# Optimization experiments

Hardware: AMD Instinct MI355X
Metric: run time of the kernel (lower is better)

## Reference

```python
import jax, jax.numpy as jnp
import numpy as np

RGB2GRAY = jnp.array([0.299, 0.587, 0.114], dtype=jnp.float32)


def _trilinear_slice(grid, z, y, x):
    """grid: (F, L, GH, GW); z,y,x: (H, W) float positions in index space
    (align_corners=True convention). Returns (H, W, F)."""
    F_, L, GH, GW = grid.shape
    z = jnp.clip(z, 0.0, L - 1)
    y = jnp.clip(y, 0.0, GH - 1)
    x = jnp.clip(x, 0.0, GW - 1)
    z0 = jnp.floor(z).astype(jnp.int32); z1 = jnp.minimum(z0 + 1, L - 1)
    y0 = jnp.floor(y).astype(jnp.int32); y1 = jnp.minimum(y0 + 1, GH - 1)
    x0 = jnp.floor(x).astype(jnp.int32); x1 = jnp.minimum(x0 + 1, GW - 1)
    wz = (z - z0)[..., None]  # (H, W, 1)
    wy = (y - y0)[..., None]
    wx = (x - x0)[..., None]

    def g(zi, yi, xi):  # gather corner -> (H, W, F)
        return jnp.moveaxis(grid[:, zi, yi, xi], 0, -1)

    c00 = g(z0, y0, x0) * (1 - wx) + g(z0, y0, x1) * wx
    c01 = g(z0, y1, x0) * (1 - wx) + g(z0, y1, x1) * wx
    c10 = g(z1, y0, x0) * (1 - wx) + g(z1, y0, x1) * wx
    c11 = g(z1, y1, x0) * (1 - wx) + g(z1, y1, x1) * wx
    c0 = c00 * (1 - wy) + c01 * wy
    c1 = c10 * (1 - wy) + c11 * wy
    return c0 * (1 - wz) + c1 * wz


def setup_inputs() -> dict:
    key = jax.random.key(0)
    k = jax.random.split(key, 5)
    H, W = 1080, 1920
    N, F_, L, GH, GW = 50, 16, 8, 16, 16
    hidden = 64
    rgb = jax.random.uniform(k[0], (H, W, 3), dtype=jnp.float32)
    grids = jax.random.normal(k[1], (N, F_, L, GH, GW), dtype=jnp.float32) * 0.1
    W1 = jax.random.normal(k[2], (hidden, F_), dtype=jnp.float32) * (1.0 / np.sqrt(F_))
    W2 = jax.random.normal(k[3], (hidden, hidden), dtype=jnp.float32) * (1.0 / np.sqrt(hidden))
    W3 = jax.random.normal(k[4], (12, hidden), dtype=jnp.float32) * (1.0 / np.sqrt(hidden))
    return {"rgb": rgb, "grids": grids, "W1": W1, "W2": W2, "W3": W3, "cam_idx": 3}


def reference(rgb, grids, W1, W2, W3, cam_idx):
    H, W, _ = rgb.shape
    _, F_, L, GH, GW = grids.shape
    grid = grids[cam_idx]  # (F, L, GH, GW)
    # guidance: gray in [0,1]; grid_sample coords in [-1,1] with align_corners=True
    # map directly to index space: pos = coord01 * (size - 1)
    gray = jnp.clip(jnp.tensordot(rgb, RGB2GRAY, axes=([-1], [0])), 0.0, 1.0)  # (H, W)
    gy = jnp.linspace(0.0, 1.0, H, dtype=jnp.float32)[:, None]  # (H, 1)
    gx = jnp.linspace(0.0, 1.0, W, dtype=jnp.float32)[None, :]  # (1, W)
    z = gray * (L - 1)
    y = jnp.broadcast_to(gy * (GH - 1), (H, W))
    x = jnp.broadcast_to(gx * (GW - 1), (H, W))
    feat = _trilinear_slice(grid, z, y, x)  # (H, W, F)
    # tiny per-pixel MLP (bias-free, torch Linear applies x @ W.T)
    h = jnp.tanh(feat @ W1.T)
    h = jnp.tanh(h @ W2.T)
    out = h @ W3.T  # (H, W, 12)
    return out.reshape(1, H, W, 3, 4)
```

## Files before the change

### kernel.cpp

```cpp
#include <hip/hip_runtime.h>

#define H_IMG 1080
#define W_IMG 1920
#define NPIX (H_IMG * W_IMG)

typedef __attribute__((ext_vector_type(8))) short bfrag8;
typedef __attribute__((ext_vector_type(4))) float facc4;

#define PK2_OFF 131072
#define PK3_OFF 147456
#define PK1_OFF 151552

__device__ __forceinline__ void split_bf16(float x, unsigned short& hi, unsigned short& lo) {
    unsigned xu = __float_as_uint(x);
    hi = (unsigned short)(xu >> 16);
    float hif = __uint_as_float(xu & 0xffff0000u);
    float lof = x - hif;
    lo = (unsigned short)(__float_as_uint(lof) >> 16);
}

__global__ void prep_kernel(const float* __restrict__ grids,
                            const int* __restrict__ cam_idx,
                            const float* __restrict__ W1,
                            const float* __restrict__ W2,
                            const float* __restrict__ W3,
                            float* __restrict__ grid_t,
                            unsigned short* __restrict__ pk1,
                            unsigned short* __restrict__ pk2,
                            unsigned short* __restrict__ pk3) {
    int idx = blockIdx.x * 256 + threadIdx.x;
    {
        int f = idx & 15, x = (idx >> 4) & 15, y = (idx >> 8) & 15, z = (idx >> 12) & 7;
        int cam = cam_idx[0];
        grid_t[idx] = grids[(((cam * 16 + f) * 8 + z) * 16 + y) * 16 + x];
    }
    if (idx < 8192) {
        int i = idx & 7, lane = (idx >> 3) & 63, h = (idx >> 9) & 1,
            s = (idx >> 10) & 1, mt = (idx >> 11) & 3;
        int j = mt * 16 + (lane & 15);
        int k = s * 32 + (lane >> 4) * 8 + i;
        unsigned short hi, lo;
        split_bf16(W2[j * 64 + k], hi, lo);
        pk2[idx] = h ? lo : hi;
    } else if (idx < 10240) {
        int e = idx - 8192;
        int i = e & 7, lane = (e >> 3) & 63, h = (e >> 9) & 1, s = (e >> 10) & 1;
        int c = lane & 15;
        int k = s * 32 + (lane >> 4) * 8 + i;
        float x = (c < 12) ? W3[c * 64 + k] : 0.0f;
        unsigned short hi, lo;
        split_bf16(x, hi, lo);
        pk3[e] = h ? lo : hi;
    } else if (idx < 14336) {
        int e = idx - 10240;
        int i = e & 7, lane = (e >> 3) & 63, h = (e >> 9) & 1, mt = (e >> 10) & 3;
        int j = mt * 16 + (lane & 15);
        int k = (lane >> 4) * 8 + i;
        float x = (k < 16) ? W1[j * 16 + k] : 0.0f;
        unsigned short hi, lo;
        split_bf16(x, hi, lo);
        pk1[e] = h ? lo : hi;
    }
}

__device__ __forceinline__ float fast_tanh(float x) {
    float e = exp2f(x * 2.8853900817779268f);
    return 1.0f - 2.0f * __builtin_amdgcn_rcpf(e + 1.0f);
}

__device__ __forceinline__ unsigned rtn_pair(float e, float o) {
    unsigned ue = __float_as_uint(e) + 0x8000u;
    unsigned uo = __float_as_uint(o) + 0x8000u;
    return __builtin_amdgcn_perm(uo, ue, 0x07060302u);
}

#define DS_FENCE() asm volatile("s_waitcnt lgkmcnt(0)" ::: "memory")
#define MFMA16(A, B, C) __builtin_amdgcn_mfma_f32_16x16x32_bf16((A), (B), (C), 0, 0, 0)

__global__ __launch_bounds__(256, 3)
void nbat_main(const float* __restrict__ rgb,
               const float* __restrict__ grid_t,
               const unsigned short* __restrict__ pk1,
               const unsigned short* __restrict__ pk2,
               const unsigned short* __restrict__ pk3,
               float* __restrict__ out) {
    __shared__ __align__(16) unsigned hbuf[4][1024];

    const int tid = threadIdx.x;
    const int w = tid >> 6, l = tid & 63;
    const int g = l >> 4, cc = l & 15;
    unsigned* hb = hbuf[w];
    uint4* hb4 = (uint4*)hb;

    const int pixbase = blockIdx.x * 256 + w * 64;
    const int pix = pixbase + l;
    const int row = pix / W_IMG;
    const int col = pix - row * W_IMG;

    float r = rgb[3 * pix + 0];
    float gch = rgb[3 * pix + 1];
    float b = rgb[3 * pix + 2];
    float gray = fminf(fmaxf(0.299f * r + 0.587f * gch + 0.114f * b, 0.0f), 1.0f);

    float z = fminf(fmaxf(gray * 7.0f, 0.0f), 7.0f);
    float y = (float)row * (15.0f / 1079.0f);
    float x = (float)col * (15.0f / 1919.0f);

    float zf = floorf(z), yf = floorf(y), xf = floorf(x);
    int z0 = (int)zf, y0 = (int)yf, x0 = (int)xf;
    int z1 = min(z0 + 1, 7), y1 = min(y0 + 1, 15), x1 = min(x0 + 1, 15);
    float wz = z - zf, wy = y - yf, wx = x - xf;

    float feat[16];
#pragma unroll
    for (int i = 0; i < 16; ++i) feat[i] = 0.0f;

    const float4* gt4 = (const float4*)grid_t;
#pragma unroll
    for (int cz = 0; cz < 2; ++cz) {
        int zz = cz ? z1 : z0;
        float wwz = cz ? wz : (1.0f - wz);
#pragma unroll
        for (int cy = 0; cy < 2; ++cy) {
            int yy = cy ? y1 : y0;
            float wwzy = wwz * (cy ? wy : (1.0f - wy));
#pragma unroll
            for (int cx = 0; cx < 2; ++cx) {
                int xx = cx ? x1 : x0;
                float wc = wwzy * (cx ? wx : (1.0f - wx));
                int base = ((zz * 16 + yy) * 16 + xx) * 4;
#pragma unroll
                for (int q = 0; q < 4; ++q) {
                    float4 v = gt4[base + q];
                    feat[4 * q + 0] = fmaf(wc, v.x, feat[4 * q + 0]);
                    feat[4 * q + 1] = fmaf(wc, v.y, feat[4 * q + 1]);
                    feat[4 * q + 2] = fmaf(wc, v.z, feat[4 * q + 2]);
                    feat[4 * q + 3] = fmaf(wc, v.w, feat[4 * q + 3]);
                }
            }
        }
    }

    const int sl = (l >> 1) & 3;
    {
        uint4 q0, q1;
        q0.x = rtn_pair(feat[0], feat[1]);
        q0.y = rtn_pair(feat[2], feat[3]);
        q0.z = rtn_pair(feat[4], feat[5]);
        q0.w = rtn_pair(feat[6], feat[7]);
        q1.x = rtn_pair(feat[8], feat[9]);
        q1.y = rtn_pair(feat[10], feat[11]);
        q1.z = rtn_pair(feat[12], feat[13]);
        q1.w = rtn_pair(feat[14], feat[15]);
        uint4 zz4 = make_uint4(0u, 0u, 0u, 0u);
        hb4[l * 4 + (0 ^ sl)] = q0;
        hb4[l * 4 + (1 ^ sl)] = q1;
        hb4[l * 4 + (2 ^ sl)] = zz4;
        hb4[l * 4 + (3 ^ sl)] = zz4;
    }
    DS_FENCE();

    auto transition = [&](const facc4& v, int mtl, int nt) __attribute__((always_inline)) {
        float t0 = fast_tanh(v[0]);
        float t1 = fast_tanh(v[1]);
        float t2 = fast_tanh(v[2]);
        float t3 = fast_tanh(v[3]);
        unsigned A = rtn_pair(t0, t1);
        unsigned B = rtn_pair(t2, t3);
        int p = cc + 16 * nt;
        int u = p * 16 + ((((mtl << 1) + (g >> 1)) ^ ((p >> 1) & 3)) << 2) + ((g & 1) << 1);
        *(uint2*)(hb + u) = make_uint2(A, B);
    };

    const bfrag8* pk1v = (const bfrag8*)pk1;
    facc4 acc1[4][4];
#pragma unroll
    for (int mt = 0; mt < 4; ++mt)
#pragma unroll
        for (int nt = 0; nt < 4; ++nt) acc1[mt][nt] = (facc4){0.f, 0.f, 0.f, 0.f};
    {
        bfrag8 w1h[4], w1l[4];
#pragma unroll
        for (int mt = 0; mt < 4; ++mt) {
            w1h[mt] = pk1v[(mt * 2 + 0) * 64 + l];
            w1l[mt] = pk1v[(mt * 2 + 1) * 64 + l];
        }
#pragma unroll
        for (int nt = 0; nt < 4; ++nt) {
            int p = cc + 16 * nt;
            uint4 bq = hb4[p * 4 + (g ^ ((p >> 1) & 3))];
            bfrag8 bf = __builtin_bit_cast(bfrag8, bq);
#pragma unroll
            for (int mt = 0; mt < 4; ++mt) {
                acc1[mt][nt] = MFMA16(w1l[mt], bf, acc1[mt][nt]);
                acc1[mt][nt] = MFMA16(w1h[mt], bf, acc1[mt][nt]);
            }
        }
    }
    DS_FENCE();

    const bfrag8* pk2v = (const bfrag8*)pk2;
    facc4 acc2[4][4];
#pragma unroll
    for (int mt = 0; mt < 4; ++mt)
#pragma unroll
        for (int nt = 0; nt < 4; ++nt) acc2[mt][nt] = (facc4){0.f, 0.f, 0.f, 0.f};

#pragma unroll
    for (int s = 0; s < 2; ++s) {
#pragma unroll
        for (int mtl = 0; mtl < 2; ++mtl)
#pragma unroll
            for (int nt = 0; nt < 4; ++nt) transition(acc1[2 * s + mtl][nt], mtl, nt);
        DS_FENCE();
        bfrag8 w2h[4], w2l[4];
#pragma unroll
        for (int mt = 0; mt < 4; ++mt) {
            w2h[mt] = pk2v[((mt * 2 + s) * 2 + 0) * 64 + l];
            w2l[mt] = pk2v[((mt * 2 + s) * 2 + 1) * 64 + l];
        }
#pragma unroll
        for (int nt = 0; nt < 4; ++nt) {
            int p = cc + 16 * nt;
            int sw = (p >> 1) & 3;
            uint4 qh = hb4[p * 4 + (g ^ sw)];
            bfrag8 bh = __builtin_bit_cast(bfrag8, qh);
#pragma unroll
            for (int mt = 0; mt < 4; ++mt) {
                acc2[mt][nt] = MFMA16(w2l[mt], bh, acc2[mt][nt]);
                acc2[mt][nt] = MFMA16(w2h[mt], bh, acc2[mt][nt]);
            }
        }
        DS_FENCE();
    }

    const bfrag8* pk3v = (const bfrag8*)pk3;
    facc4 o3[4];
#pragma unroll
    for (int nt = 0; nt < 4; ++nt) o3[nt] = (facc4){0.f, 0.f, 0.f, 0.f};

#pragma unroll
    for (int s = 0; s < 2; ++s) {
#pragma unroll
        for (int mtl = 0; mtl < 2; ++mtl)
#pragma unroll
            for (int nt = 0; nt < 4; ++nt) transition(acc2[2 * s + mtl][nt], mtl, nt);
        DS_FENCE();
        bfrag8 w3h = pk3v[(s * 2 + 0) * 64 + l];
        bfrag8 w3l = pk3v[(s * 2 + 1) * 64 + l];
#pragma unroll
        for (int nt = 0; nt < 4; ++nt) {
            int p = cc + 16 * nt;
            int sw = (p >> 1) & 3;
            uint4 qh = hb4[p * 4 + (g ^ sw)];
            bfrag8 bh = __builtin_bit_cast(bfrag8, qh);
            o3[nt] = MFMA16(w3l, bh, o3[nt]);
            o3[nt] = MFMA16(w3h, bh, o3[nt]);
        }
        if (s == 0) DS_FENCE();
    }

    if (g < 3) {
#pragma unroll
        for (int nt = 0; nt < 4; ++nt) {
            int p = pixbase + 16 * nt + cc;
            *(float4*)(out + p * 12 + 4 * g) =
                make_float4(o3[nt][0], o3[nt][1], o3[nt][2], o3[nt][3]);
        }
    }
}

extern "C" void kernel_launch(void* const* d_in, const int* in_sizes, int n_in,
                              void* d_out, int out_size, void* d_ws, size_t ws_size,
                              hipStream_t stream) {
    const float* rgb   = (const float*)d_in[0];
    const float* grids = (const float*)d_in[1];
    const float* W1    = (const float*)d_in[2];
    const float* W2    = (const float*)d_in[3];
    const float* W3    = (const float*)d_in[4];
    const int*   cam   = (const int*)d_in[5];

    float* grid_t = (float*)d_ws;
    unsigned short* pk2 = (unsigned short*)((char*)d_ws + PK2_OFF);
    unsigned short* pk3 = (unsigned short*)((char*)d_ws + PK3_OFF);
    unsigned short* pk1 = (unsigned short*)((char*)d_ws + PK1_OFF);

    hipLaunchKernelGGL(prep_kernel, dim3(128), dim3(256), 0, stream,
                       grids, cam, W1, W2, W3, grid_t, pk1, pk2, pk3);
    hipLaunchKernelGGL(nbat_main, dim3(NPIX / 256), dim3(256), 0, stream,
                       rgb, grid_t, pk1, pk2, pk3, (float*)d_out);
}
```

Before: 155.3 us.

## Split layer-2/3 MLP into pixel halves with a larger LDS staging buffer

Layer 1's full 64-wide tanh activations are written to a separate LDS region (3x larger per-wave buffer), so the layer-1 accumulators are released early. Layers 2 and 3 then run over two halves of 32 pixels each, which halves the live acc2/o3 accumulator registers and removes the per-k-slice fence interleaving. The aim is lower register pressure and fewer LDS round-trip stalls. In exchange it uses 48KB of LDS per block, which may limit occupancy, and the swizzle layout is changed to match.

```diff
diff --git a/kernel.cpp b/kernel.cpp
--- a/kernel.cpp
+++ b/kernel.cpp
@@ -75,6 +75,7 @@
 }
 
 #define DS_FENCE() asm volatile("s_waitcnt lgkmcnt(0)" ::: "memory")
+#define CBAR() asm volatile("" ::: "memory")
 #define MFMA16(A, B, C) __builtin_amdgcn_mfma_f32_16x16x32_bf16((A), (B), (C), 0, 0, 0)
 
 __global__ __launch_bounds__(256, 3)
@@ -84,13 +85,14 @@
                const unsigned short* __restrict__ pk2,
                const unsigned short* __restrict__ pk3,
                float* __restrict__ out) {
-    __shared__ __align__(16) unsigned hbuf[4][1024];
+    __shared__ __align__(16) unsigned hbuf[4][3072];
 
     const int tid = threadIdx.x;
     const int w = tid >> 6, l = tid & 63;
     const int g = l >> 4, cc = l & 15;
     unsigned* hb = hbuf[w];
     uint4* hb4 = (uint4*)hb;
+    const int H4 = 256;
 
     const int pixbase = blockIdx.x * 256 + w * 64;
     const int pix = pixbase + l;
@@ -160,15 +162,16 @@
     }
     DS_FENCE();
 
-    auto transition = [&](const facc4& v, int mtl, int nt) __attribute__((always_inline)) {
+    auto trans = [&](const facc4& v, int mt, int prow, int ubase)
+        __attribute__((always_inline)) {
         float t0 = fast_tanh(v[0]);
         float t1 = fast_tanh(v[1]);
         float t2 = fast_tanh(v[2]);
         float t3 = fast_tanh(v[3]);
         unsigned A = rtn_pair(t0, t1);
         unsigned B = rtn_pair(t2, t3);
-        int p = cc + 16 * nt;
-        int u = p * 16 + ((((mtl << 1) + (g >> 1)) ^ ((p >> 1) & 3)) << 2) + ((g & 1) << 1);
+        int c = 2 * mt + (g >> 1);
+        int u = ubase + prow * 32 + (((c ^ (prow & 7)) << 2) + ((g & 1) << 1));
         *(uint2*)(hb + u) = make_uint2(A, B);
     };
 
@@ -197,76 +200,75 @@
             }
         }
     }
+
+#pragma unroll
+    for (int mt = 0; mt < 4; ++mt)
+#pragma unroll
+        for (int nt = 0; nt < 4; ++nt) trans(acc1[mt][nt], mt, cc + 16 * nt, 1024);
     DS_FENCE();
 
     const bfrag8* pk2v = (const bfrag8*)pk2;
-    facc4 acc2[4][4];
-#pragma unroll
-    for (int mt = 0; mt < 4; ++mt)
-#pragma unroll
-        for (int nt = 0; nt < 4; ++nt) acc2[mt][nt] = (facc4){0.f, 0.f, 0.f, 0.f};
-
-#pragma unroll
-    for (int s = 0; s < 2; ++s) {
-#pragma unroll
-        for (int mtl = 0; mtl < 2; ++mtl)
-#pragma unroll
-            for (int nt = 0; nt < 4; ++nt) transition(acc1[2 * s + mtl][nt], mtl, nt);
+    const bfrag8* pk3v = (const bfrag8*)pk3;
+#pragma unroll
+    for (int h = 0; h < 2; ++h) {
+        facc4 acc2[4][2];
+#pragma unroll
+        for (int mt = 0; mt < 4; ++mt)
+#pragma unroll
+            for (int ntl = 0; ntl < 2; ++ntl) acc2[mt][ntl] = (facc4){0.f, 0.f, 0.f, 0.f};
+#pragma unroll
+        for (int s = 0; s < 2; ++s) {
+            bfrag8 w2h[4], w2l[4];
+#pragma unroll
+            for (int mt = 0; mt < 4; ++mt) {
+                w2h[mt] = pk2v[((mt * 2 + s) * 2 + 0) * 64 + l];
+                w2l[mt] = pk2v[((mt * 2 + s) * 2 + 1) * 64 + l];
+            }
+#pragma unroll
+            for (int ntl = 0; ntl < 2; ++ntl) {
+                int p = cc + 16 * (2 * h + ntl);
+                uint4 q = hb4[H4 + p * 8 + ((4 * s + g) ^ (p & 7))];
+                bfrag8 bh = __builtin_bit_cast(bfrag8, q);
+#pragma unroll
+                for (int mt = 0; mt < 4; ++mt) {
+                    acc2[mt][ntl] = MFMA16(w2l[mt], bh, acc2[mt][ntl]);
+                    acc2[mt][ntl] = MFMA16(w2h[mt], bh, acc2[mt][ntl]);
+                }
+            }
+        }
+
+#pragma unroll
+        for (int mt = 0; mt < 4; ++mt)
+#pragma unroll
+            for (int ntl = 0; ntl < 2; ++ntl) trans(acc2[mt][ntl], mt, cc + 16 * ntl, 0);
         DS_FENCE();
-        bfrag8 w2h[4], w2l[4];
-#pragma unroll
-        for (int mt = 0; mt < 4; ++mt) {
-            w2h[mt] = pk2v[((mt * 2 + s) * 2 + 0) * 64 + l];
-            w2l[mt] = pk2v[((mt * 2 + s) * 2 + 1) * 64 + l];
-        }
-#pragma unroll
-        for (int nt = 0; nt < 4; ++nt) {
-            int p = cc + 16 * nt;
-            int sw = (p >> 1) & 3;
-            uint4 qh = hb4[p * 4 + (g ^ sw)];
-            bfrag8 bh = __builtin_bit_cast(bfrag8, qh);
-#pragma unroll
-            for (int mt = 0; mt < 4; ++mt) {
-                acc2[mt][nt] = MFMA16(w2l[mt], bh, acc2[mt][nt]);
-                acc2[mt][nt] = MFMA16(w2h[mt], bh, acc2[mt][nt]);
-            }
-        }
-        DS_FENCE();
-    }
-
-    const bfrag8* pk3v = (const bfrag8*)pk3;
-    facc4 o3[4];
-#pragma unroll
-    for (int nt = 0; nt < 4; ++nt) o3[nt] = (facc4){0.f, 0.f, 0.f, 0.f};
-
-#pragma unroll
-    for (int s = 0; s < 2; ++s) {
-#pragma unroll
-        for (int mtl = 0; mtl < 2; ++mtl)
-#pragma unroll
-            for (int nt = 0; nt < 4; ++nt) transition(acc2[2 * s + mtl][nt], mtl, nt);
-        DS_FENCE();
-        bfrag8 w3h = pk3v[(s * 2 + 0) * 64 + l];
-        bfrag8 w3l = pk3v[(s * 2 + 1) * 64 + l];
-#pragma unroll
-        for (int nt = 0; nt < 4; ++nt) {
-            int p = cc + 16 * nt;
-            int sw = (p >> 1) & 3;
-            uint4 qh = hb4[p * 4 + (g ^ sw)];
-            bfrag8 bh = __builtin_bit_cast(bfrag8, qh);
-            o3[nt] = MFMA16(w3l, bh, o3[nt]);
-            o3[nt] = MFMA16(w3h, bh, o3[nt]);
-        }
-        if (s == 0) DS_FENCE();
-    }
-
-    if (g < 3) {
-#pragma unroll
-        for (int nt = 0; nt < 4; ++nt) {
-            int p = pixbase + 16 * nt + cc;
-            *(float4*)(out + p * 12 + 4 * g) =
-                make_float4(o3[nt][0], o3[nt][1], o3[nt][2], o3[nt][3]);
-        }
+
+        facc4 o3[2];
+#pragma unroll
+        for (int ntl = 0; ntl < 2; ++ntl) o3[ntl] = (facc4){0.f, 0.f, 0.f, 0.f};
+#pragma unroll
+        for (int s = 0; s < 2; ++s) {
+            bfrag8 w3h = pk3v[(s * 2 + 0) * 64 + l];
+            bfrag8 w3l = pk3v[(s * 2 + 1) * 64 + l];
+#pragma unroll
+            for (int ntl = 0; ntl < 2; ++ntl) {
+                int pl = cc + 16 * ntl;
+                uint4 q = hb4[pl * 8 + ((4 * s + g) ^ (pl & 7))];
+                bfrag8 bh = __builtin_bit_cast(bfrag8, q);
+                o3[ntl] = MFMA16(w3l, bh, o3[ntl]);
+                o3[ntl] = MFMA16(w3h, bh, o3[ntl]);
+            }
+        }
+
+        if (g < 3) {
+#pragma unroll
+            for (int ntl = 0; ntl < 2; ++ntl) {
+                int p = pixbase + 32 * h + 16 * ntl + cc;
+                *(float4*)(out + p * 12 + 4 * g) =
+                    make_float4(o3[ntl][0], o3[ntl][1], o3[ntl][2], o3[ntl][3]);
+            }
+        }
+        CBAR();
     }
 }
 
```

Result: slower. 181.7 us (+17.0%).
